# Performance work log

Measured on AMD Instinct MI355X. Metric: run time of the kernel, lower is better.

## Reference

```python
import jax, jax.numpy as jnp
import numpy as np

B, T, D_MODEL, D_HEAD = 4, 4096, 512, 64  # batch, token_depth, token_len, d_head
D_K = 64
NEG = -1.0e9  # mask fill value used by the torch module


def setup_inputs() -> dict:
    key = jax.random.key(0)
    kx, kq, kk, kv = jax.random.split(key, 4)
    x = jax.random.normal(kx, (B, T, D_MODEL), dtype=jnp.float32)
    # nn.Linear(token_len, d_head, bias=False) -> weight shape [d_head, token_len]
    Wq = jax.random.normal(kq, (D_HEAD, D_MODEL), dtype=jnp.float32) * 0.02
    Wk = jax.random.normal(kk, (D_HEAD, D_MODEL), dtype=jnp.float32) * 0.02
    Wv = jax.random.normal(kv, (D_HEAD, D_MODEL), dtype=jnp.float32) * 0.02
    return {"x": x, "Wq": Wq, "Wk": Wk, "Wv": Wv}


def reference(x, Wq, Wk, Wv):
    # q/k/v projections: y = x @ W.T  (Linear with bias=False)
    q = jnp.einsum("btd,hd->bth", x, Wq)  # [B,T,D_HEAD]
    k = jnp.einsum("btd,hd->bth", x, Wk)
    v = jnp.einsum("btd,hd->bth", x, Wv)

    scores = jnp.einsum("bth,bsh->bts", q, k)  # [B,T,T]

    # additive causal mask: upper triangle (diagonal=1) filled with -1e9
    t_idx = jnp.arange(T)
    mask = jnp.where(t_idx[None, :] > t_idx[:, None], NEG, 0.0).astype(scores.dtype)
    scores = scores + mask[None, :, :]

    sqrt_dk = jnp.sqrt(jnp.asarray(D_K, dtype=scores.dtype))
    # NOTE: original code applies softmax over dim=1 (the query axis), not -1.
    attn = jax.nn.softmax(scores / sqrt_dk, axis=1)
    out = jnp.einsum("bts,bsh->bth", attn, v)  # [B,T,D_HEAD]
    return out
```

## Files before the change

kernel.cpp:

```cpp
#include <hip/hip_runtime.h>

#define B_ 4
#define T_ 4096
#define DM 512
#define DH 64
#define CS 512
#define CTS 512

typedef short short8 __attribute__((ext_vector_type(8)));
typedef short bf16x4 __attribute__((ext_vector_type(4)));
typedef float f32x4 __attribute__((ext_vector_type(4)));
typedef float float8 __attribute__((ext_vector_type(8)));

__device__ inline short f2bf(float f) {
    unsigned u = __float_as_uint(f);
    u += 0x7fffu + ((u >> 16) & 1u);
    return (short)(u >> 16);
}
__device__ inline float bf2f(short s) {
    return __uint_as_float(((unsigned)(unsigned short)s) << 16);
}
__device__ inline short8 cvt8(const float* p) {
    float8 v = *(const float8*)p;
    short8 r;
#pragma unroll
    for (int j = 0; j < 8; j++) r[j] = f2bf(v[j]);
    return r;
}
__device__ inline unsigned cvt_pk_bf16(float a, float b) {
    unsigned r;
    asm("v_cvt_pk_bf16_f32 %0, %1, %2" : "=v"(r) : "v"(a), "v"(b));
    return r;
}
__device__ inline bf16x4 pmask4(f32x4 d, int sbase, int t) {
    float p[4];
#pragma unroll
    for (int r = 0; r < 4; r++) {
        float e = __expf(d[r] * 0.125f);
        p[r] = (sbase + r <= t) ? e : 0.f;
    }
    union { unsigned u[2]; bf16x4 v; } z;
    z.u[0] = cvt_pk_bf16(p[0], p[1]);
    z.u[1] = cvt_pk_bf16(p[2], p[3]);
    return z.v;
}

__global__ __launch_bounds__(256) void k_wcvt(
    const float* __restrict__ Wq, const float* __restrict__ Wk,
    const float* __restrict__ Wv, short* __restrict__ wb)
{
    int e = (blockIdx.x * 256 + threadIdx.x) * 8;
    int m = e / (DH * DM);
    int off = e - m * (DH * DM);
    const float* W = (m == 0) ? Wq : (m == 1) ? Wk : Wv;
    *(short8*)(wb + e) = cvt8(W + off);
}

__global__ __launch_bounds__(256, 4) void k_proj(
    const float* __restrict__ x, const short* __restrict__ wb,
    short* __restrict__ qb, short* __restrict__ kb, short* __restrict__ vb)
{
    __shared__ short Xs[16 * 72];
    __shared__ short Ws[192 * 72];
    int tid = threadIdx.x;
    int lane = tid & 63, w = tid >> 6;
    int l16 = lane & 15, quad = lane >> 4;
    int b = blockIdx.x >> 8;
    int tile = blockIdx.x & 255;
    int t0 = tile * 16;
    long xbase = ((long)(b * T_ + t0)) * DM;
    int hb = w * 3;

    f32x4 acc[3];
#pragma unroll
    for (int i = 0; i < 3; i++) acc[i] = (f32x4)(0.f);

    for (int kc = 0; kc < DM; kc += 64) {
        if (tid < 128) {
            int row = tid >> 3, col = (tid & 7) * 8;
            *(short8*)(Xs + row * 72 + col) = cvt8(x + xbase + (long)row * DM + kc + col);
        }
#pragma unroll
        for (int p = 0; p < 6; p++) {
            int idx = p * 256 + tid;
            int row = idx >> 3, col = (idx & 7) * 8;
            *(short8*)(Ws + row * 72 + col) =
                *(const short8*)(wb + (long)row * DM + kc + col);
        }
        __syncthreads();
#pragma unroll
        for (int ks = 0; ks < 2; ks++) {
            short8 af = *(const short8*)(Xs + l16 * 72 + ks * 32 + quad * 8);
#pragma unroll
            for (int j = 0; j < 3; j++) {
                short8 bf = *(const short8*)(Ws + ((hb + j) * 16 + l16) * 72 + ks * 32 + quad * 8);
                acc[j] = __builtin_amdgcn_mfma_f32_16x16x32_bf16(af, bf, acc[j], 0, 0, 0);
            }
        }
        __syncthreads();
    }
#pragma unroll
    for (int j = 0; j < 3; j++) {
        int hh = hb + j, m = hh >> 2, h4 = hh & 3;
        short* outp = (m == 0) ? qb : (m == 1) ? kb : vb;
#pragma unroll
        for (int r4 = 0; r4 < 4; r4++) {
            int t = t0 + quad * 4 + r4;
            outp[((long)(b * T_ + t)) * DH + h4 * 16 + l16] = f2bf(acc[j][r4]);
        }
    }
}

__global__ __launch_bounds__(256, 4) void k_stats(
    const short* __restrict__ qb, const short* __restrict__ kb, float* __restrict__ lsum)
{
    __shared__ short Qb[128 * 72];
    int tid = threadIdx.x;
    int lane = tid & 63, w = tid >> 6;
    int l16 = lane & 15, quad = lane >> 4;
    const int NC = T_ / CTS;
    int chunk = blockIdx.x % NC;
    int st = (blockIdx.x / NC) & 31;
    int b = blockIdx.x / (NC * 32);
    int c0 = chunk * CTS, cend = c0 + CTS;
    int s0blk = st * 128;
    if (cend <= s0blk) return;
    int s0w = s0blk + w * 32;
    long bq = (long)b * T_ * DH;

    const short8* kp0 = (const short8*)(kb + bq + (long)(s0w + l16) * DH + quad * 8);
    short8 a00 = kp0[0], a01 = kp0[4];
    const short8* kp1 = (const short8*)(kb + bq + (long)(s0w + 16 + l16) * DH + quad * 8);
    short8 a10 = kp1[0], a11 = kp1[4];

    int t_lo = (c0 > s0blk) ? c0 : s0blk;
    int nsteps = (cend - t_lo) >> 7;
    float acc0[4] = {0.f, 0.f, 0.f, 0.f};
    float acc1[4] = {0.f, 0.f, 0.f, 0.f};

    for (int stp = 0; stp < nsteps; stp++) {
        int t0 = t_lo + stp * 128;
#pragma unroll
        for (int p = 0; p < 4; p++) {
            int idx = p * 256 + tid;
            int row = idx >> 3, col = idx & 7;
            *(short8*)(Qb + row * 72 + col * 8) =
                *(const short8*)(qb + bq + (long)(t0 + row) * DH + col * 8);
        }
        __syncthreads();
        for (int sub = 0; sub < 8; sub++) {
            int tt = t0 + sub * 16;
            if (tt + 15 >= s0w) {
                short8 b0 = *(const short8*)(Qb + (sub * 16 + l16) * 72 + quad * 8);
                short8 b1 = *(const short8*)(Qb + (sub * 16 + l16) * 72 + 32 + quad * 8);
                int t = tt + l16;
                f32x4 d0 = (f32x4)(0.f);
                d0 = __builtin_amdgcn_mfma_f32_16x16x32_bf16(a00, b0, d0, 0, 0, 0);
                d0 = __builtin_amdgcn_mfma_f32_16x16x32_bf16(a01, b1, d0, 0, 0, 0);
#pragma unroll
                for (int r = 0; r < 4; r++) {
                    int s = s0w + quad * 4 + r;
                    float p = __expf(d0[r] * 0.125f);
                    acc0[r] += (t >= s) ? p : 0.f;
                }
                if (tt + 15 >= s0w + 16) {
                    f32x4 d1 = (f32x4)(0.f);
                    d1 = __builtin_amdgcn_mfma_f32_16x16x32_bf16(a10, b0, d1, 0, 0, 0);
                    d1 = __builtin_amdgcn_mfma_f32_16x16x32_bf16(a11, b1, d1, 0, 0, 0);
#pragma unroll
                    for (int r = 0; r < 4; r++) {
                        int s = s0w + 16 + quad * 4 + r;
                        float p = __expf(d1[r] * 0.125f);
                        acc1[r] += (t >= s) ? p : 0.f;
                    }
                }
            }
        }
        __syncthreads();
    }
#pragma unroll
    for (int r = 0; r < 4; r++) {
        float v = acc0[r];
        v += __shfl_xor(v, 1, 16); v += __shfl_xor(v, 2, 16);
        v += __shfl_xor(v, 4, 16); v += __shfl_xor(v, 8, 16);
        if (l16 == 0) atomicAdd(&lsum[b * T_ + s0w + quad * 4 + r], v);
        float v1 = acc1[r];
        v1 += __shfl_xor(v1, 1, 16); v1 += __shfl_xor(v1, 2, 16);
        v1 += __shfl_xor(v1, 4, 16); v1 += __shfl_xor(v1, 8, 16);
        if (l16 == 0) atomicAdd(&lsum[b * T_ + s0w + 16 + quad * 4 + r], v1);
    }
}

__global__ __launch_bounds__(256) void k_vt(
    const short* __restrict__ vb, const float* __restrict__ lsum, short* __restrict__ vTc)
{
    int tid = threadIdx.x;
    int b = blockIdx.x >> 6;
    int s0 = (blockIdx.x & 63) * 64;
    int h = tid & 63, g = tid >> 6;
    long vbase = ((long)(b * T_) + s0 + g * 16) * DH + h;
    long lbase = (long)b * T_ + s0 + g * 16;
    short8 lo, hi;
#pragma unroll
    for (int k2 = 0; k2 < 8; k2++) {
        float rl = 1.0f / lsum[lbase + k2];
        lo[k2] = f2bf(bf2f(vb[vbase + (long)k2 * DH]) * rl);
        float rh = 1.0f / lsum[lbase + 8 + k2];
        hi[k2] = f2bf(bf2f(vb[vbase + (long)(8 + k2) * DH]) * rh);
    }
    long ob = ((long)(b * 256 + (s0 >> 4) + g) * 64 + h) * 16;
    *(short8*)(vTc + ob) = lo;
    *(short8*)(vTc + ob + 8) = hi;
}

__global__ __launch_bounds__(256, 4) void k_out(
    const short* __restrict__ qb, const short* __restrict__ kb,
    const short* __restrict__ vTc, float* __restrict__ out)
{
    __shared__ short Kb[128 * 72];
    int tid = threadIdx.x;
    int lane = tid & 63, w = tid >> 6;
    int l16 = lane & 15, quad = lane >> 4;
    const int NC = T_ / CS;
    int chunk = blockIdx.x % NC;
    int strip = (blockIdx.x / NC) & 31;
    int b = blockIdx.x / (NC * 32);
    int c0 = chunk * CS;
    int blk_tmax = strip * 128 + 127;
    if (c0 > blk_tmax) return;
    int s_hi = (c0 + CS < blk_tmax + 1) ? c0 + CS : blk_tmax + 1;
    int nsteps = (s_hi - c0 + 127) >> 7;
    int t0w = strip * 128 + w * 32;
    long bq = (long)b * T_ * DH;

    const short8* qp0 = (const short8*)(qb + bq + (long)(t0w + l16) * DH + quad * 8);
    short8 q00 = qp0[0], q01 = qp0[4];
    const short8* qp1 = (const short8*)(qb + bq + (long)(t0w + 16 + l16) * DH + quad * 8);
    short8 q10 = qp1[0], q11 = qp1[4];
    const short* vTb = vTc + (long)b * (T_ / 16) * DH * 16;

    f32x4 o0[4], o1[4];
#pragma unroll
    for (int i = 0; i < 4; i++) { o0[i] = (f32x4)(0.f); o1[i] = (f32x4)(0.f); }
    int t0 = t0w + l16, t1 = t0 + 16;

    for (int stp = 0; stp < nsteps; stp++) {
        int s0 = c0 + stp * 128;
#pragma unroll
        for (int p = 0; p < 4; p++) {
            int idx = p * 256 + tid;
            int row = idx >> 3, col = idx & 7;
            *(short8*)(Kb + row * 72 + col * 8) =
                *(const short8*)(kb + bq + (long)(s0 + row) * DH + col * 8);
        }
        __syncthreads();

        for (int sub = 0; sub < 8; sub++) {
            int sc = s0 + sub * 16;
            if (sc > t0w + 31) break;
            short8 a0 = *(const short8*)(Kb + (sub * 16 + l16) * 72 + quad * 8);
            short8 a1 = *(const short8*)(Kb + (sub * 16 + l16) * 72 + 32 + quad * 8);

            f32x4 d1 = (f32x4)(0.f);
            d1 = __builtin_amdgcn_mfma_f32_16x16x32_bf16(a0, q10, d1, 0, 0, 0);
            d1 = __builtin_amdgcn_mfma_f32_16x16x32_bf16(a1, q11, d1, 0, 0, 0);
            bf16x4 pa1 = pmask4(d1, sc + quad * 4, t1);

            bf16x4 pa0 = (bf16x4)(short)0;
            if (sc <= t0w + 15) {
                f32x4 d0 = (f32x4)(0.f);
                d0 = __builtin_amdgcn_mfma_f32_16x16x32_bf16(a0, q00, d0, 0, 0, 0);
                d0 = __builtin_amdgcn_mfma_f32_16x16x32_bf16(a1, q01, d0, 0, 0, 0);
                pa0 = pmask4(d0, sc + quad * 4, t0);
            }
            const short* vc = vTb + (long)((sc) >> 4) * 1024 + quad * 4;
#pragma unroll
            for (int h4 = 0; h4 < 4; h4++) {
                bf16x4 bv = *(const bf16x4*)(vc + (h4 * 16 + l16) * 16);
                o1[h4] = __builtin_amdgcn_mfma_f32_16x16x16bf16_1k(pa1, bv, o1[h4], 0, 0, 0);
                o0[h4] = __builtin_amdgcn_mfma_f32_16x16x16bf16_1k(pa0, bv, o0[h4], 0, 0, 0);
            }
        }
        __syncthreads();
    }
#pragma unroll
    for (int h4 = 0; h4 < 4; h4++)
#pragma unroll
        for (int r = 0; r < 4; r++) {
            int t = t0w + quad * 4 + r;
            atomicAdd(&out[bq + (long)t * DH + h4 * 16 + l16], o0[h4][r]);
            atomicAdd(&out[bq + (long)(t + 16) * DH + h4 * 16 + l16], o1[h4][r]);
        }
}

extern "C" void kernel_launch(void* const* d_in, const int* in_sizes, int n_in,
                              void* d_out, int out_size, void* d_ws, size_t ws_size,
                              hipStream_t stream) {
    const float* x  = (const float*)d_in[0];
    const float* Wq = (const float*)d_in[1];
    const float* Wk = (const float*)d_in[2];
    const float* Wv = (const float*)d_in[3];
    float* out = (float*)d_out;

    char* ws = (char*)d_ws;
    short* qb   = (short*)(ws);
    short* kb   = (short*)(ws + (2l << 20));
    short* vb   = (short*)(ws + (4l << 20));
    short* vTc  = (short*)(ws + (6l << 20));
    short* wb   = (short*)(ws + (8l << 20));
    float* lsum = (float*)(ws + (9l << 20));

    hipMemsetAsync(out, 0, (size_t)out_size * sizeof(float), stream);
    hipMemsetAsync(lsum, 0, (size_t)(B_ * T_) * sizeof(float), stream);

    k_wcvt<<<dim3(48), dim3(256), 0, stream>>>(Wq, Wk, Wv, wb);
    k_proj<<<dim3(B_ * T_ / 16), dim3(256), 0, stream>>>(x, wb, qb, kb, vb);
    k_stats<<<dim3(B_ * 32 * (T_ / CTS)), dim3(256), 0, stream>>>(qb, kb, lsum);
    k_vt<<<dim3(B_ * T_ / 64), dim3(256), 0, stream>>>(vb, lsum, vTc);
    k_out<<<dim3(B_ * 32 * (T_ / CS)), dim3(256), 0, stream>>>(qb, kb, vTc, out);
}
```

Measured before the change: 150.3 us.

## Prefetch next Q/K tile into registers, hoist V loads, halve chunk size

Both the column-sum kernel and the output kernel now load the next 128-row Q or K tile from global memory into registers while the current tile is being processed, then store it to LDS at the start of the next step. V fragment loads are hoisted ahead of the QK MFMAs so their latency overlaps compute. Chunk sizes CS/CTS drop from 512 to 256, which launches more blocks for better parallelism but adds more atomic adds and partial-sum work per output. Holding the prefetched tile in registers raises register pressure.

```diff
diff --git a/kernel.cpp b/kernel.cpp
--- a/kernel.cpp
+++ b/kernel.cpp
@@ -4,8 +4,8 @@
 #define T_ 4096
 #define DM 512
 #define DH 64
-#define CS 512
-#define CTS 512
+#define CS 256
+#define CTS 256
 
 typedef short short8 __attribute__((ext_vector_type(8)));
 typedef short bf16x4 __attribute__((ext_vector_type(4)));
@@ -138,14 +138,22 @@
     float acc0[4] = {0.f, 0.f, 0.f, 0.f};
     float acc1[4] = {0.f, 0.f, 0.f, 0.f};
 
+    int srow = tid >> 3, scol = (tid & 7) * 8;
+    short8 rg[4];
+#pragma unroll
+    for (int p = 0; p < 4; p++)
+        rg[p] = *(const short8*)(qb + bq + (long)(t_lo + p * 32 + srow) * DH + scol);
+
     for (int stp = 0; stp < nsteps; stp++) {
         int t0 = t_lo + stp * 128;
 #pragma unroll
-        for (int p = 0; p < 4; p++) {
-            int idx = p * 256 + tid;
-            int row = idx >> 3, col = idx & 7;
-            *(short8*)(Qb + row * 72 + col * 8) =
-                *(const short8*)(qb + bq + (long)(t0 + row) * DH + col * 8);
+        for (int p = 0; p < 4; p++)
+            *(short8*)(Qb + (p * 32 + srow) * 72 + scol) = rg[p];
+        if (stp + 1 < nsteps) {
+            int tn = t0 + 128;
+#pragma unroll
+            for (int p = 0; p < 4; p++)
+                rg[p] = *(const short8*)(qb + bq + (long)(tn + p * 32 + srow) * DH + scol);
         }
         __syncthreads();
         for (int sub = 0; sub < 8; sub++) {
@@ -244,14 +252,22 @@
     for (int i = 0; i < 4; i++) { o0[i] = (f32x4)(0.f); o1[i] = (f32x4)(0.f); }
     int t0 = t0w + l16, t1 = t0 + 16;
 
+    int srow = tid >> 3, scol = (tid & 7) * 8;
+    short8 rg[4];
+#pragma unroll
+    for (int p = 0; p < 4; p++)
+        rg[p] = *(const short8*)(kb + bq + (long)(c0 + p * 32 + srow) * DH + scol);
+
     for (int stp = 0; stp < nsteps; stp++) {
         int s0 = c0 + stp * 128;
 #pragma unroll
-        for (int p = 0; p < 4; p++) {
-            int idx = p * 256 + tid;
-            int row = idx >> 3, col = idx & 7;
-            *(short8*)(Kb + row * 72 + col * 8) =
-                *(const short8*)(kb + bq + (long)(s0 + row) * DH + col * 8);
+        for (int p = 0; p < 4; p++)
+            *(short8*)(Kb + (p * 32 + srow) * 72 + scol) = rg[p];
+        if (stp + 1 < nsteps) {
+            int sn = s0 + 128;
+#pragma unroll
+            for (int p = 0; p < 4; p++)
+                rg[p] = *(const short8*)(kb + bq + (long)(sn + p * 32 + srow) * DH + scol);
         }
         __syncthreads();
 
@@ -260,6 +276,11 @@
             if (sc > t0w + 31) break;
             short8 a0 = *(const short8*)(Kb + (sub * 16 + l16) * 72 + quad * 8);
             short8 a1 = *(const short8*)(Kb + (sub * 16 + l16) * 72 + 32 + quad * 8);
+            const short* vc = vTb + (long)(sc >> 4) * 1024 + quad * 4;
+            bf16x4 bv[4];
+#pragma unroll
+            for (int h4 = 0; h4 < 4; h4++)
+                bv[h4] = *(const bf16x4*)(vc + (h4 * 16 + l16) * 16);
 
             f32x4 d1 = (f32x4)(0.f);
             d1 = __builtin_amdgcn_mfma_f32_16x16x32_bf16(a0, q10, d1, 0, 0, 0);
@@ -273,12 +294,10 @@
                 d0 = __builtin_amdgcn_mfma_f32_16x16x32_bf16(a1, q01, d0, 0, 0, 0);
                 pa0 = pmask4(d0, sc + quad * 4, t0);
             }
-            const short* vc = vTb + (long)((sc) >> 4) * 1024 + quad * 4;
 #pragma unroll
             for (int h4 = 0; h4 < 4; h4++) {
-                bf16x4 bv = *(const bf16x4*)(vc + (h4 * 16 + l16) * 16);
-                o1[h4] = __builtin_amdgcn_mfma_f32_16x16x16bf16_1k(pa1, bv, o1[h4], 0, 0, 0);
-                o0[h4] = __builtin_amdgcn_mfma_f32_16x16x16bf16_1k(pa0, bv, o0[h4], 0, 0, 0);
+                o1[h4] = __builtin_amdgcn_mfma_f32_16x16x16bf16_1k(pa1, bv[h4], o1[h4], 0, 0, 0);
+                o0[h4] = __builtin_amdgcn_mfma_f32_16x16x16bf16_1k(pa0, bv[h4], o0[h4], 0, 0, 0);
             }
         }
         __syncthreads();
```

Result: slower. 153.5 us (+2.2%).

## Fold weight conversion and buffer zeroing into projection/stats kernels, prefetch V

Applied to the files above, without the earlier changes.

Removes the separate weight-conversion kernel and both memset calls. k_proj now converts fp32 weights to bf16 while staging them, and zeroes the lsum buffer. k_stats zeroes the output buffer before it returns early, which is safe because k_out runs later in the same stream. The V fragment loads in k_out are hoisted ahead of the QK MFMAs so memory latency overlaps compute. The aim is to cut launch and memset overhead, at the cost of redundant fp32 weight reads and conversions in every proj block.

```diff
diff --git a/kernel.cpp b/kernel.cpp
--- a/kernel.cpp
+++ b/kernel.cpp
@@ -45,20 +45,11 @@
     return z.v;
 }
 
-__global__ __launch_bounds__(256) void k_wcvt(
-    const float* __restrict__ Wq, const float* __restrict__ Wk,
-    const float* __restrict__ Wv, short* __restrict__ wb)
-{
-    int e = (blockIdx.x * 256 + threadIdx.x) * 8;
-    int m = e / (DH * DM);
-    int off = e - m * (DH * DM);
-    const float* W = (m == 0) ? Wq : (m == 1) ? Wk : Wv;
-    *(short8*)(wb + e) = cvt8(W + off);
-}
-
 __global__ __launch_bounds__(256, 4) void k_proj(
-    const float* __restrict__ x, const short* __restrict__ wb,
-    short* __restrict__ qb, short* __restrict__ kb, short* __restrict__ vb)
+    const float* __restrict__ x, const float* __restrict__ Wq,
+    const float* __restrict__ Wk, const float* __restrict__ Wv,
+    short* __restrict__ qb, short* __restrict__ kb, short* __restrict__ vb,
+    float* __restrict__ lsum)
 {
     __shared__ short Xs[16 * 72];
     __shared__ short Ws[192 * 72];
@@ -71,6 +62,8 @@
     long xbase = ((long)(b * T_ + t0)) * DM;
     int hb = w * 3;
 
+    if (tid < 16) lsum[blockIdx.x * 16 + tid] = 0.f;
+
     f32x4 acc[3];
 #pragma unroll
     for (int i = 0; i < 3; i++) acc[i] = (f32x4)(0.f);
@@ -84,8 +77,8 @@
         for (int p = 0; p < 6; p++) {
             int idx = p * 256 + tid;
             int row = idx >> 3, col = (idx & 7) * 8;
-            *(short8*)(Ws + row * 72 + col) =
-                *(const short8*)(wb + (long)row * DM + kc + col);
+            const float* Wsrc = (p < 2) ? Wq : (p < 4) ? Wk : Wv;
+            *(short8*)(Ws + row * 72 + col) = cvt8(Wsrc + (long)(row & 63) * DM + kc + col);
         }
         __syncthreads();
 #pragma unroll
@@ -112,12 +105,16 @@
 }
 
 __global__ __launch_bounds__(256, 4) void k_stats(
-    const short* __restrict__ qb, const short* __restrict__ kb, float* __restrict__ lsum)
+    const short* __restrict__ qb, const short* __restrict__ kb,
+    float* __restrict__ lsum, float* __restrict__ out)
 {
     __shared__ short Qb[128 * 72];
     int tid = threadIdx.x;
     int lane = tid & 63, w = tid >> 6;
     int l16 = lane & 15, quad = lane >> 4;
+
+    *(f32x4*)(out + ((long)blockIdx.x * 256 + tid) * 4) = (f32x4)(0.f);
+
     const int NC = T_ / CTS;
     int chunk = blockIdx.x % NC;
     int st = (blockIdx.x / NC) & 31;
@@ -260,6 +257,11 @@
             if (sc > t0w + 31) break;
             short8 a0 = *(const short8*)(Kb + (sub * 16 + l16) * 72 + quad * 8);
             short8 a1 = *(const short8*)(Kb + (sub * 16 + l16) * 72 + 32 + quad * 8);
+            const short* vc = vTb + (long)(sc >> 4) * 1024 + quad * 4;
+            bf16x4 bv[4];
+#pragma unroll
+            for (int h4 = 0; h4 < 4; h4++)
+                bv[h4] = *(const bf16x4*)(vc + (h4 * 16 + l16) * 16);
 
             f32x4 d1 = (f32x4)(0.f);
             d1 = __builtin_amdgcn_mfma_f32_16x16x32_bf16(a0, q10, d1, 0, 0, 0);
@@ -273,12 +275,10 @@
                 d0 = __builtin_amdgcn_mfma_f32_16x16x32_bf16(a1, q01, d0, 0, 0, 0);
                 pa0 = pmask4(d0, sc + quad * 4, t0);
             }
-            const short* vc = vTb + (long)((sc) >> 4) * 1024 + quad * 4;
 #pragma unroll
             for (int h4 = 0; h4 < 4; h4++) {
-                bf16x4 bv = *(const bf16x4*)(vc + (h4 * 16 + l16) * 16);
-                o1[h4] = __builtin_amdgcn_mfma_f32_16x16x16bf16_1k(pa1, bv, o1[h4], 0, 0, 0);
-                o0[h4] = __builtin_amdgcn_mfma_f32_16x16x16bf16_1k(pa0, bv, o0[h4], 0, 0, 0);
+                o1[h4] = __builtin_amdgcn_mfma_f32_16x16x16bf16_1k(pa1, bv[h4], o1[h4], 0, 0, 0);
+                o0[h4] = __builtin_amdgcn_mfma_f32_16x16x16bf16_1k(pa0, bv[h4], o0[h4], 0, 0, 0);
             }
         }
         __syncthreads();
@@ -307,15 +307,10 @@
     short* kb   = (short*)(ws + (2l << 20));
     short* vb   = (short*)(ws + (4l << 20));
     short* vTc  = (short*)(ws + (6l << 20));
-    short* wb   = (short*)(ws + (8l << 20));
-    float* lsum = (float*)(ws + (9l << 20));
-
-    hipMemsetAsync(out, 0, (size_t)out_size * sizeof(float), stream);
-    hipMemsetAsync(lsum, 0, (size_t)(B_ * T_) * sizeof(float), stream);
-
-    k_wcvt<<<dim3(48), dim3(256), 0, stream>>>(Wq, Wk, Wv, wb);
-    k_proj<<<dim3(B_ * T_ / 16), dim3(256), 0, stream>>>(x, wb, qb, kb, vb);
-    k_stats<<<dim3(B_ * 32 * (T_ / CTS)), dim3(256), 0, stream>>>(qb, kb, lsum);
+    float* lsum = (float*)(ws + (8l << 20));
+
+    k_proj<<<dim3(B_ * T_ / 16), dim3(256), 0, stream>>>(x, Wq, Wk, Wv, qb, kb, vb, lsum);
+    k_stats<<<dim3(B_ * 32 * (T_ / CTS)), dim3(256), 0, stream>>>(qb, kb, lsum, out);
     k_vt<<<dim3(B_ * T_ / 64), dim3(256), 0, stream>>>(vb, lsum, vTc);
     k_out<<<dim3(B_ * 32 * (T_ / CS)), dim3(256), 0, stream>>>(qb, kb, vTc, out);
 }
```

Measured after the change: 150.9 us. No clear change (+0.4%).
